# Kernel tuning notes

Hardware: AMD Instinct MI355X
Metric: run time of the kernel (lower is better)

Reference implementation:

```python
import jax, jax.numpy as jnp
import numpy as np

B, S, C = 4, 2048, 1024
N_HEAD = 16
HEAD_DIM = C // N_HEAD


def setup_inputs() -> dict:
    key = jax.random.key(0)
    k1, k2, k3, k4, k5 = jax.random.split(key, 5)
    scale = 1.0 / np.sqrt(C)
    x = jax.random.normal(k1, (B, S, C), dtype=jnp.float32)
    W_attn = jax.random.normal(k2, (C, 3 * C), dtype=jnp.float32) * scale
    b_attn = jax.random.normal(k3, (3 * C,), dtype=jnp.float32) * 0.02
    W_proj = jax.random.normal(k4, (C, C), dtype=jnp.float32) * scale
    b_proj = jax.random.normal(k5, (C,), dtype=jnp.float32) * 0.02
    return {"x": x, "W_attn": W_attn, "b_attn": b_attn, "W_proj": W_proj, "b_proj": b_proj}


def reference(x, W_attn, b_attn, W_proj, b_proj):
    Bx, Sx, Cx = x.shape
    qkv = x @ W_attn + b_attn                      # [B,S,3C]
    q, k, v = jnp.split(qkv, 3, axis=-1)
    # [B,S,C] -> [B,H,S,D]
    def heads(t):
        return t.reshape(Bx, Sx, N_HEAD, HEAD_DIM).transpose(0, 2, 1, 3)
    q, k, v = heads(q), heads(k), heads(v)
    scores = jnp.einsum('bhqd,bhkd->bhqk', q, k) / np.sqrt(HEAD_DIM)
    causal = jnp.tril(jnp.ones((Sx, Sx), dtype=bool))
    scores = jnp.where(causal[None, None], scores, -jnp.inf)
    attn = jax.nn.softmax(scores, axis=-1)
    out = jnp.einsum('bhqk,bhkd->bhqd', attn, v)   # [B,H,S,D]
    out = out.transpose(0, 2, 1, 3).reshape(Bx, Sx, Cx)
    return out @ W_proj + b_proj
```

## Files before the change

### kernel.cpp

```cpp
#include <hip/hip_runtime.h>
#include <hip/hip_bf16.h>

typedef __hip_bfloat16 bf16;
#define NEG_BIG (-3.0e38f)

typedef __bf16 bf16x8 __attribute__((ext_vector_type(8)));
typedef float  f32x4  __attribute__((ext_vector_type(4)));

__device__ inline void load8_f32(const float* p, float* o) {
  float4 a = *reinterpret_cast<const float4*>(p);
  float4 b = *reinterpret_cast<const float4*>(p + 4);
  o[0]=a.x; o[1]=a.y; o[2]=a.z; o[3]=a.w;
  o[4]=b.x; o[5]=b.y; o[6]=b.z; o[7]=b.w;
}

__device__ inline int swz8(int row, int kg) { return ((kg ^ ((row >> 3) & 3)) << 3); }

__global__ __launch_bounds__(1024)
void qkv_f(const float* __restrict__ X, const float* __restrict__ W,
           const float* __restrict__ bias,
           bf16* __restrict__ q, bf16* __restrict__ k, bf16* __restrict__ v)
{
  __shared__ __align__(16) unsigned char smem[67584];
  bf16 (*As)[40] = reinterpret_cast<bf16 (*)[40]>(smem);
  bf16 (*Bs)[48] = reinterpret_cast<bf16 (*)[48]>(smem + 40960);

  const int t   = threadIdx.x;
  const int f   = blockIdx.x;
  const int xcd = f & 7, j = f >> 3;
  const int bm  = xcd * 4 + (j & 3);
  const int bn  = j >> 2;
  const int gm0 = bm * 256, gn0 = bn * 128;
  const int w    = t >> 6, lane = t & 63;
  const int g    = lane >> 4, l15 = lane & 15;
  const int wr   = w >> 2, wc = w & 3;

  const int am  = t >> 2, akg = t & 3;
  const int bnr = t & 127, kg4 = t >> 7;

  f32x4 acc[4][2];
#pragma unroll
  for (int i = 0; i < 4; i++)
#pragma unroll
    for (int jj = 0; jj < 2; jj++) acc[i][jj] = {0.f, 0.f, 0.f, 0.f};

  const float* aptr = X + (size_t)(gm0 + am) * 1024 + akg * 8;
  const float* wptr = W + (size_t)(kg4 * 4) * 3072 + gn0 + bnr;

  float a32_0[8], a32_1[8], wb_0[4], wb_1[4];
  load8_f32(aptr, a32_0);
#pragma unroll
  for (int kk = 0; kk < 4; kk++) wb_0[kk] = wptr[kk * 3072];
  aptr += 32; wptr += 32 * 3072;
  load8_f32(aptr, a32_1);
#pragma unroll
  for (int kk = 0; kk < 4; kk++) wb_1[kk] = wptr[kk * 3072];

  for (int kt = 0; kt < 1024; kt += 64) {
    {
      __align__(16) bf16 ab[8];
      __align__(8)  bf16 bb[4];
#pragma unroll
      for (int i = 0; i < 8; i++) ab[i] = __float2bfloat16(a32_0[i]);
#pragma unroll
      for (int i = 0; i < 4; i++) bb[i] = __float2bfloat16(wb_0[i]);
      *reinterpret_cast<uint4*>(&As[am][swz8(am, akg)]) = *reinterpret_cast<const uint4*>(ab);
      *reinterpret_cast<uint2*>(&Bs[bnr][swz8(bnr, kg4 >> 1) + (kg4 & 1) * 4]) =
          *reinterpret_cast<const uint2*>(bb);
      if (kt + 64 < 1024) {
        aptr += 32; wptr += 32 * 3072;
        load8_f32(aptr, a32_0);
#pragma unroll
        for (int kk = 0; kk < 4; kk++) wb_0[kk] = wptr[kk * 3072];
      }
      __syncthreads();
      bf16x8 af[4], bfr[2];
#pragma unroll
      for (int mt = 0; mt < 4; mt++) {
        const int r_ = wr * 64 + mt * 16 + l15;
        af[mt] = *reinterpret_cast<const bf16x8*>(&As[r_][swz8(r_, g)]);
      }
#pragma unroll
      for (int nt = 0; nt < 2; nt++) {
        const int r_ = wc * 32 + nt * 16 + l15;
        bfr[nt] = *reinterpret_cast<const bf16x8*>(&Bs[r_][swz8(r_, g)]);
      }
      __builtin_amdgcn_s_setprio(1);
#pragma unroll
      for (int mt = 0; mt < 4; mt++)
#pragma unroll
        for (int nt = 0; nt < 2; nt++)
          acc[mt][nt] = __builtin_amdgcn_mfma_f32_16x16x32_bf16(af[mt], bfr[nt], acc[mt][nt], 0, 0, 0);
      __builtin_amdgcn_s_setprio(0);
    }
    {
      __align__(16) bf16 ab[8];
      __align__(8)  bf16 bb[4];
#pragma unroll
      for (int i = 0; i < 8; i++) ab[i] = __float2bfloat16(a32_1[i]);
#pragma unroll
      for (int i = 0; i < 4; i++) bb[i] = __float2bfloat16(wb_1[i]);
      *reinterpret_cast<uint4*>(&As[256 + am][swz8(am, akg)]) = *reinterpret_cast<const uint4*>(ab);
      *reinterpret_cast<uint2*>(&Bs[128 + bnr][swz8(bnr, kg4 >> 1) + (kg4 & 1) * 4]) =
          *reinterpret_cast<const uint2*>(bb);
      if (kt + 96 < 1024) {
        aptr += 32; wptr += 32 * 3072;
        load8_f32(aptr, a32_1);
#pragma unroll
        for (int kk = 0; kk < 4; kk++) wb_1[kk] = wptr[kk * 3072];
      }
      __syncthreads();
      bf16x8 af[4], bfr[2];
#pragma unroll
      for (int mt = 0; mt < 4; mt++) {
        const int r_ = wr * 64 + mt * 16 + l15;
        af[mt] = *reinterpret_cast<const bf16x8*>(&As[256 + r_][swz8(r_, g)]);
      }
#pragma unroll
      for (int nt = 0; nt < 2; nt++) {
        const int r_ = wc * 32 + nt * 16 + l15;
        bfr[nt] = *reinterpret_cast<const bf16x8*>(&Bs[128 + r_][swz8(r_, g)]);
      }
      __builtin_amdgcn_s_setprio(1);
#pragma unroll
      for (int mt = 0; mt < 4; mt++)
#pragma unroll
        for (int nt = 0; nt < 2; nt++)
          acc[mt][nt] = __builtin_amdgcn_mfma_f32_16x16x32_bf16(af[mt], bfr[nt], acc[mt][nt], 0, 0, 0);
      __builtin_amdgcn_s_setprio(0);
    }
  }

  const int which = gn0 >> 10;
  if (which == 2) {
    bf16 (*Vep)[264] = reinterpret_cast<bf16 (*)[264]>(smem);
    __syncthreads();
#pragma unroll
    for (int nt = 0; nt < 2; nt++) {
      const int c = wc * 32 + nt * 16 + l15;
      const float bvs = bias[gn0 + c];
#pragma unroll
      for (int mt = 0; mt < 4; mt++)
#pragma unroll
        for (int r = 0; r < 4; r++) {
          const int s = wr * 64 + mt * 16 + g * 4 + r;
          Vep[c][s] = __float2bfloat16(acc[mt][nt][r] + bvs);
        }
    }
    __syncthreads();
    const int c   = t >> 3, tl = t & 7;
    const int bb2 = gm0 >> 11, sl0 = gm0 & 2047;
    const int hh  = ((gn0 - 2048) >> 6) + (c >> 6), d = c & 63;
    bf16* vrow = v + ((size_t)(bb2 * 16 + hh) * 64 + d) * 2048 + sl0;
#pragma unroll
    for (int it = 0; it < 4; it++) {
      const int s_off = tl * 8 + it * 64;
      *reinterpret_cast<uint4*>(vrow + s_off) =
          *reinterpret_cast<const uint4*>(&Vep[c][s_off]);
    }
  } else {
    bf16* dst = (which == 0) ? q : k;
#pragma unroll
    for (int nt = 0; nt < 2; nt++) {
      const int gc  = gn0 + wc * 32 + nt * 16 + l15;
      const float bvs = bias[gc];
      const int cc = gc & 1023;
      const int hh = cc >> 6, d = cc & 63;
#pragma unroll
      for (int mt = 0; mt < 4; mt++)
#pragma unroll
        for (int r = 0; r < 4; r++) {
          const int gr = gm0 + wr * 64 + mt * 16 + g * 4 + r;
          const int bb2 = gr >> 11, s = gr & 2047;
          float val = acc[mt][nt][r] + bvs;
          if (which == 0) val *= 0.125f;
          dst[((size_t)(bb2 * 16 + hh) * 2048 + s) * 64 + d] = __float2bfloat16(val);
        }
    }
  }
}

__global__ __launch_bounds__(256)
void attn_f(bf16* __restrict__ qo, const bf16* __restrict__ k, const bf16* __restrict__ v)
{
  __shared__ __align__(16) bf16 Ks[64][72];
  __shared__ __align__(16) bf16 Vt[64][72];
  __shared__ __align__(16) bf16 Ps[4][16][72];

  const int t    = threadIdx.x;
  const int f    = blockIdx.x;
  const int xcd  = f & 7;
  const int j    = f >> 3;
  const int hb   = xcd + 8 * (j >> 4);
  const int qt0  = j & 15;
  const int b    = hb >> 4, h = hb & 15;
  const size_t basebh = (size_t)(b * 16 + h) * 2048 * 64;

  const int w    = t >> 6;
  const int lane = t & 63;
  const int g    = lane >> 4;
  const int l15  = lane & 15;

  const int sr = t >> 3;
  const int sc = (t & 7) * 8;
  const bf16* kbase = k + basebh;
  const bf16* vbase = v + basebh;

#pragma unroll 1
  for (int pass = 0; pass < 2; ++pass) {
    const int qt = pass ? qt0 : (31 - qt0);
    const int qb = qt * 64 + w * 16;

    const bf16* qrow = qo + basebh + (size_t)(qb + l15) * 64;
    bf16x8 qf0 = *reinterpret_cast<const bf16x8*>(qrow + g * 8);
    bf16x8 qf1 = *reinterpret_cast<const bf16x8*>(qrow + 32 + g * 8);

    f32x4 acc[4] = {{0,0,0,0},{0,0,0,0},{0,0,0,0},{0,0,0,0}};
    float m_run = NEG_BIG, l_run = 0.f;

    uint4 kreg0, kreg1, vreg0, vreg1;
    {
      kreg0 = *reinterpret_cast<const uint4*>(kbase + (size_t)(sr) * 64 + sc);
      kreg1 = *reinterpret_cast<const uint4*>(kbase + (size_t)(32 + sr) * 64 + sc);
      vreg0 = *reinterpret_cast<const uint4*>(vbase + (size_t)sr * 2048 + sc);
      vreg1 = *reinterpret_cast<const uint4*>(vbase + (size_t)(32 + sr) * 2048 + sc);
    }

    for (int ct = 0; ct <= qt; ++ct) {
      const int kv0 = ct * 64;
      __syncthreads();
      *reinterpret_cast<uint4*>(&Ks[sr][sc])      = kreg0;
      *reinterpret_cast<uint4*>(&Ks[32 + sr][sc]) = kreg1;
      *reinterpret_cast<uint4*>(&Vt[sr][sc])      = vreg0;
      *reinterpret_cast<uint4*>(&Vt[32 + sr][sc]) = vreg1;
      if (ct < qt) {
        const int nv0 = kv0 + 64;
        kreg0 = *reinterpret_cast<const uint4*>(kbase + (size_t)(nv0 + sr) * 64 + sc);
        kreg1 = *reinterpret_cast<const uint4*>(kbase + (size_t)(nv0 + 32 + sr) * 64 + sc);
        vreg0 = *reinterpret_cast<const uint4*>(vbase + (size_t)sr * 2048 + nv0 + sc);
        vreg1 = *reinterpret_cast<const uint4*>(vbase + (size_t)(32 + sr) * 2048 + nv0 + sc);
      }
      __syncthreads();

      f32x4 st[4];
      __builtin_amdgcn_s_setprio(1);
#pragma unroll
      for (int kt = 0; kt < 4; ++kt) {
        const int kr = kt * 16 + l15;
        bf16x8 kf0 = *reinterpret_cast<const bf16x8*>(&Ks[kr][g * 8]);
        bf16x8 kf1 = *reinterpret_cast<const bf16x8*>(&Ks[kr][32 + g * 8]);
        f32x4 c4 = {0,0,0,0};
        c4 = __builtin_amdgcn_mfma_f32_16x16x32_bf16(kf0, qf0, c4, 0, 0, 0);
        c4 = __builtin_amdgcn_mfma_f32_16x16x32_bf16(kf1, qf1, c4, 0, 0, 0);
        st[kt] = c4;
      }
      __builtin_amdgcn_s_setprio(0);
      if (ct == qt) {
        const int qg = qb + l15;
#pragma unroll
        for (int kt = 0; kt < 4; ++kt)
#pragma unroll
          for (int r = 0; r < 4; ++r)
            if (kv0 + kt * 16 + g * 4 + r > qg) st[kt][r] = NEG_BIG;
      }

      float mc = NEG_BIG;
#pragma unroll
      for (int kt = 0; kt < 4; ++kt)
#pragma unroll
        for (int r = 0; r < 4; ++r) mc = fmaxf(mc, st[kt][r]);
      mc = fmaxf(mc, __shfl_xor(mc, 16));
      mc = fmaxf(mc, __shfl_xor(mc, 32));
      if (!__all(mc - m_run <= 8.0f)) {
        const float mn = fmaxf(m_run, mc);
        const float alpha = __expf(m_run - mn);
        m_run = mn;
        l_run *= alpha;
#pragma unroll
        for (int r = 0; r < 4; ++r) {
          const float ar = __shfl(alpha, g * 4 + r, 64);
#pragma unroll
          for (int dt = 0; dt < 4; ++dt) acc[dt][r] *= ar;
        }
      }
      float ps = 0.f;
#pragma unroll
      for (int kt = 0; kt < 4; ++kt)
#pragma unroll
        for (int r = 0; r < 4; ++r) {
          const float pv = __expf(st[kt][r] - m_run);
          st[kt][r] = pv;
          ps += pv;
        }
      ps += __shfl_xor(ps, 16);
      ps += __shfl_xor(ps, 32);
      l_run += ps;

#pragma unroll
      for (int kt = 0; kt < 4; ++kt) {
        union { bf16 hh[4]; uint2 u; } pk;
        pk.hh[0] = __float2bfloat16(st[kt][0]);
        pk.hh[1] = __float2bfloat16(st[kt][1]);
        pk.hh[2] = __float2bfloat16(st[kt][2]);
        pk.hh[3] = __float2bfloat16(st[kt][3]);
        *reinterpret_cast<uint2*>(&Ps[w][l15][kt * 16 + g * 4]) = pk.u;
      }
      __builtin_amdgcn_sched_barrier(0);

      __builtin_amdgcn_s_setprio(1);
#pragma unroll
      for (int kc = 0; kc < 2; ++kc) {
        bf16x8 pf = *reinterpret_cast<const bf16x8*>(&Ps[w][l15][kc * 32 + g * 8]);
#pragma unroll
        for (int dt = 0; dt < 4; ++dt) {
          bf16x8 vf = *reinterpret_cast<const bf16x8*>(&Vt[dt * 16 + l15][kc * 32 + g * 8]);
          acc[dt] = __builtin_amdgcn_mfma_f32_16x16x32_bf16(pf, vf, acc[dt], 0, 0, 0);
        }
      }
      __builtin_amdgcn_s_setprio(0);
    }

    const float linv = 1.f / l_run;
    float inv[4];
#pragma unroll
    for (int r = 0; r < 4; ++r) inv[r] = __shfl(linv, g * 4 + r, 64);
    bf16* op = qo + basebh;
#pragma unroll
    for (int dt = 0; dt < 4; ++dt)
#pragma unroll
      for (int r = 0; r < 4; ++r)
        op[(size_t)(qb + g * 4 + r) * 64 + dt * 16 + l15] =
            __float2bfloat16(acc[dt][r] * inv[r]);
  }
}

__global__ __launch_bounds__(1024)
void proj_f(const bf16* __restrict__ A, const float* __restrict__ W,
            const float* __restrict__ bias, float* __restrict__ out)
{
  __shared__ __align__(16) bf16 As[2][256][40];
  __shared__ __align__(16) bf16 Bs[2][128][48];
  const int t   = threadIdx.x;
  const int f   = blockIdx.x;
  const int xcd = f & 7, j = f >> 3;
  const int bm  = xcd * 4 + (j & 3);
  const int bn  = j >> 2;
  const int gm0 = bm * 256, gn0 = bn * 128;
  const int w    = t >> 6, lane = t & 63;
  const int g    = lane >> 4, l15 = lane & 15;
  const int wr   = w >> 2, wc = w & 3;

  const int am  = t >> 2, akg = t & 3;
  const int bnr = t & 127, kg4 = t >> 7;

  const int gr_l = gm0 + am;
  const int bb_l = gr_l >> 11, s_l = gr_l & 2047;
  const bf16* abase = A + (size_t)bb_l * 2097152 + (size_t)s_l * 64;

  f32x4 acc[4][2];
#pragma unroll
  for (int i = 0; i < 4; i++)
#pragma unroll
    for (int jj = 0; jj < 2; jj++) acc[i][jj] = {0.f, 0.f, 0.f, 0.f};

  const float* wptr = W + (size_t)(kg4 * 4) * 1024 + gn0 + bnr;

  uint4 a0_0, a0_1;
  float wb_0[4], wb_1[4];
  {
    const int c0 = akg * 8;
    a0_0 = *reinterpret_cast<const uint4*>(abase + (size_t)(c0 >> 6) * 131072 + (c0 & 63));
    const int c1 = 32 + akg * 8;
    a0_1 = *reinterpret_cast<const uint4*>(abase + (size_t)(c1 >> 6) * 131072 + (c1 & 63));
  }
#pragma unroll
  for (int kk = 0; kk < 4; kk++) wb_0[kk] = wptr[kk * 1024];
  wptr += 32 * 1024;
#pragma unroll
  for (int kk = 0; kk < 4; kk++) wb_1[kk] = wptr[kk * 1024];

  for (int kt = 0; kt < 1024; kt += 64) {
    {
      __align__(8) bf16 bb[4];
#pragma unroll
      for (int i = 0; i < 4; i++) bb[i] = __float2bfloat16(wb_0[i]);
      *reinterpret_cast<uint4*>(&As[0][am][swz8(am, akg)]) = a0_0;
      *reinterpret_cast<uint2*>(&Bs[0][bnr][swz8(bnr, kg4 >> 1) + (kg4 & 1) * 4]) =
          *reinterpret_cast<const uint2*>(bb);
      if (kt + 64 < 1024) {
        const int c0 = kt + 64 + akg * 8;
        a0_0 = *reinterpret_cast<const uint4*>(abase + (size_t)(c0 >> 6) * 131072 + (c0 & 63));
        wptr += 32 * 1024;
#pragma unroll
        for (int kk = 0; kk < 4; kk++) wb_0[kk] = wptr[kk * 1024];
      }
      __syncthreads();
      bf16x8 af[4], bfr[2];
#pragma unroll
      for (int mt = 0; mt < 4; mt++) {
        const int r_ = wr * 64 + mt * 16 + l15;
        af[mt] = *reinterpret_cast<const bf16x8*>(&As[0][r_][swz8(r_, g)]);
      }
#pragma unroll
      for (int nt = 0; nt < 2; nt++) {
        const int r_ = wc * 32 + nt * 16 + l15;
        bfr[nt] = *reinterpret_cast<const bf16x8*>(&Bs[0][r_][swz8(r_, g)]);
      }
      __builtin_amdgcn_s_setprio(1);
#pragma unroll
      for (int mt = 0; mt < 4; mt++)
#pragma unroll
        for (int nt = 0; nt < 2; nt++)
          acc[mt][nt] = __builtin_amdgcn_mfma_f32_16x16x32_bf16(af[mt], bfr[nt], acc[mt][nt], 0, 0, 0);
      __builtin_amdgcn_s_setprio(0);
    }
    {
      __align__(8) bf16 bb[4];
#pragma unroll
      for (int i = 0; i < 4; i++) bb[i] = __float2bfloat16(wb_1[i]);
      *reinterpret_cast<uint4*>(&As[1][am][swz8(am, akg)]) = a0_1;
      *reinterpret_cast<uint2*>(&Bs[1][bnr][swz8(bnr, kg4 >> 1) + (kg4 & 1) * 4]) =
          *reinterpret_cast<const uint2*>(bb);
      if (kt + 96 < 1024) {
        const int c1 = kt + 96 + akg * 8;
        a0_1 = *reinterpret_cast<const uint4*>(abase + (size_t)(c1 >> 6) * 131072 + (c1 & 63));
        wptr += 32 * 1024;
#pragma unroll
        for (int kk = 0; kk < 4; kk++) wb_1[kk] = wptr[kk * 1024];
      }
      __syncthreads();
      bf16x8 af[4], bfr[2];
#pragma unroll
      for (int mt = 0; mt < 4; mt++) {
        const int r_ = wr * 64 + mt * 16 + l15;
        af[mt] = *reinterpret_cast<const bf16x8*>(&As[1][r_][swz8(r_, g)]);
      }
#pragma unroll
      for (int nt = 0; nt < 2; nt++) {
        const int r_ = wc * 32 + nt * 16 + l15;
        bfr[nt] = *reinterpret_cast<const bf16x8*>(&Bs[1][r_][swz8(r_, g)]);
      }
      __builtin_amdgcn_s_setprio(1);
#pragma unroll
      for (int mt = 0; mt < 4; mt++)
#pragma unroll
        for (int nt = 0; nt < 2; nt++)
          acc[mt][nt] = __builtin_amdgcn_mfma_f32_16x16x32_bf16(af[mt], bfr[nt], acc[mt][nt], 0, 0, 0);
      __builtin_amdgcn_s_setprio(0);
    }
  }

#pragma unroll
  for (int nt = 0; nt < 2; nt++) {
    const int gc = gn0 + wc * 32 + nt * 16 + l15;
    const float bvs = bias[gc];
#pragma unroll
    for (int mt = 0; mt < 4; mt++)
#pragma unroll
      for (int r = 0; r < 4; r++) {
        const int gr = gm0 + wr * 64 + mt * 16 + g * 4 + r;
        out[(size_t)gr * 1024 + gc] = acc[mt][nt][r] + bvs;
      }
  }
}

extern "C" void kernel_launch(void* const* d_in, const int* in_sizes, int n_in,
                              void* d_out, int out_size, void* d_ws, size_t ws_size,
                              hipStream_t stream)
{
  const float *x = nullptr, *W_attn = nullptr, *b_attn = nullptr,
              *W_proj = nullptr, *b_proj = nullptr;
  for (int i = 0; i < n_in; i++) {
    switch (in_sizes[i]) {
      case 8388608: x      = (const float*)d_in[i]; break;
      case 3145728: W_attn = (const float*)d_in[i]; break;
      case 3072:    b_attn = (const float*)d_in[i]; break;
      case 1048576: W_proj = (const float*)d_in[i]; break;
      case 1024:    b_proj = (const float*)d_in[i]; break;
      default: break;
    }
  }
  if (!x || !W_attn || !b_attn || !W_proj || !b_proj) {
    x = (const float*)d_in[0]; W_attn = (const float*)d_in[1];
    b_attn = (const float*)d_in[2]; W_proj = (const float*)d_in[3];
    b_proj = (const float*)d_in[4];
  }
  float* out = (float*)d_out;

  const size_t NE = 8388608;
  bf16* qb = (bf16*)d_ws;
  bf16* kb = (bf16*)d_out;
  bf16* vb = kb + NE;

  qkv_f <<<dim3(768), 1024, 0, stream>>>(x, W_attn, b_attn, qb, kb, vb);
  attn_f<<<dim3(1024), 256, 0, stream>>>(qb, kb, vb);
  proj_f<<<dim3(256), 1024, 0, stream>>>(qb, W_proj, b_proj, out);
}
```

Measured before the change: 187.5 us.

## Process paired causal query tiles in one KV sweep sharing K/V tiles

The attention kernel used to run two sequential passes per block, one for the long query tile (31-qt0) and one for the short tile (qt0), each reloading K/V from global memory. It now sweeps the KV tiles once and feeds both query tiles from the same shared-memory K/V tile, with separate softmax state, accumulators and P buffers. This removes redundant K/V global loads and barriers for the shorter tile and adds independent MFMA work per iteration. In exchange register pressure roughly doubles; a launch_bounds occupancy hint is added and the block-to-head mapping is reordered.

```diff
diff --git a/kernel.cpp b/kernel.cpp
--- a/kernel.cpp
+++ b/kernel.cpp
@@ -180,19 +180,20 @@
   }
 }
 
-__global__ __launch_bounds__(256)
+__global__ __launch_bounds__(256, 4)
 void attn_f(bf16* __restrict__ qo, const bf16* __restrict__ k, const bf16* __restrict__ v)
 {
   __shared__ __align__(16) bf16 Ks[64][72];
   __shared__ __align__(16) bf16 Vt[64][72];
-  __shared__ __align__(16) bf16 Ps[4][16][72];
+  __shared__ __align__(16) bf16 Ps[2][4][16][72];
 
   const int t    = threadIdx.x;
   const int f    = blockIdx.x;
   const int xcd  = f & 7;
   const int j    = f >> 3;
-  const int hb   = xcd + 8 * (j >> 4);
-  const int qt0  = j & 15;
+  const int a    = j & 7;
+  const int qt0  = j >> 3;
+  const int hb   = xcd + 8 * a;
   const int b    = hb >> 4, h = hb & 15;
   const size_t basebh = (size_t)(b * 16 + h) * 2048 * 64;
 
@@ -206,42 +207,48 @@
   const bf16* kbase = k + basebh;
   const bf16* vbase = v + basebh;
 
+  const int qtA = 31 - qt0, qtB = qt0;
+  const int qbA = qtA * 64 + w * 16;
+  const int qbB = qtB * 64 + w * 16;
+
+  const bf16* qrowA = qo + basebh + (size_t)(qbA + l15) * 64;
+  bf16x8 qfA0 = *reinterpret_cast<const bf16x8*>(qrowA + g * 8);
+  bf16x8 qfA1 = *reinterpret_cast<const bf16x8*>(qrowA + 32 + g * 8);
+  const bf16* qrowB = qo + basebh + (size_t)(qbB + l15) * 64;
+  bf16x8 qfB0 = *reinterpret_cast<const bf16x8*>(qrowB + g * 8);
+  bf16x8 qfB1 = *reinterpret_cast<const bf16x8*>(qrowB + 32 + g * 8);
+
+  f32x4 accA[4] = {{0,0,0,0},{0,0,0,0},{0,0,0,0},{0,0,0,0}};
+  f32x4 accB[4] = {{0,0,0,0},{0,0,0,0},{0,0,0,0},{0,0,0,0}};
+  float mA = NEG_BIG, lA = 0.f, mB = NEG_BIG, lB = 0.f;
+
+  uint4 kreg0, kreg1, vreg0, vreg1;
+  {
+    kreg0 = *reinterpret_cast<const uint4*>(kbase + (size_t)(sr) * 64 + sc);
+    kreg1 = *reinterpret_cast<const uint4*>(kbase + (size_t)(32 + sr) * 64 + sc);
+    vreg0 = *reinterpret_cast<const uint4*>(vbase + (size_t)sr * 2048 + sc);
+    vreg1 = *reinterpret_cast<const uint4*>(vbase + (size_t)(32 + sr) * 2048 + sc);
+  }
+
 #pragma unroll 1
-  for (int pass = 0; pass < 2; ++pass) {
-    const int qt = pass ? qt0 : (31 - qt0);
-    const int qb = qt * 64 + w * 16;
-
-    const bf16* qrow = qo + basebh + (size_t)(qb + l15) * 64;
-    bf16x8 qf0 = *reinterpret_cast<const bf16x8*>(qrow + g * 8);
-    bf16x8 qf1 = *reinterpret_cast<const bf16x8*>(qrow + 32 + g * 8);
-
-    f32x4 acc[4] = {{0,0,0,0},{0,0,0,0},{0,0,0,0},{0,0,0,0}};
-    float m_run = NEG_BIG, l_run = 0.f;
-
-    uint4 kreg0, kreg1, vreg0, vreg1;
+  for (int ct = 0; ct <= qtA; ++ct) {
+    const int kv0 = ct * 64;
+    const bool doB = (ct <= qtB);
+    __syncthreads();
+    *reinterpret_cast<uint4*>(&Ks[sr][sc])      = kreg0;
+    *reinterpret_cast<uint4*>(&Ks[32 + sr][sc]) = kreg1;
+    *reinterpret_cast<uint4*>(&Vt[sr][sc])      = vreg0;
+    *reinterpret_cast<uint4*>(&Vt[32 + sr][sc]) = vreg1;
+    if (ct < qtA) {
+      const int nv0 = kv0 + 64;
+      kreg0 = *reinterpret_cast<const uint4*>(kbase + (size_t)(nv0 + sr) * 64 + sc);
+      kreg1 = *reinterpret_cast<const uint4*>(kbase + (size_t)(nv0 + 32 + sr) * 64 + sc);
+      vreg0 = *reinterpret_cast<const uint4*>(vbase + (size_t)sr * 2048 + nv0 + sc);
+      vreg1 = *reinterpret_cast<const uint4*>(vbase + (size_t)(32 + sr) * 2048 + nv0 + sc);
+    }
+    __syncthreads();
+
     {
-      kreg0 = *reinterpret_cast<const uint4*>(kbase + (size_t)(sr) * 64 + sc);
-      kreg1 = *reinterpret_cast<const uint4*>(kbase + (size_t)(32 + sr) * 64 + sc);
-      vreg0 = *reinterpret_cast<const uint4*>(vbase + (size_t)sr * 2048 + sc);
-      vreg1 = *reinterpret_cast<const uint4*>(vbase + (size_t)(32 + sr) * 2048 + sc);
-    }
-
-    for (int ct = 0; ct <= qt; ++ct) {
-      const int kv0 = ct * 64;
-      __syncthreads();
-      *reinterpret_cast<uint4*>(&Ks[sr][sc])      = kreg0;
-      *reinterpret_cast<uint4*>(&Ks[32 + sr][sc]) = kreg1;
-      *reinterpret_cast<uint4*>(&Vt[sr][sc])      = vreg0;
-      *reinterpret_cast<uint4*>(&Vt[32 + sr][sc]) = vreg1;
-      if (ct < qt) {
-        const int nv0 = kv0 + 64;
-        kreg0 = *reinterpret_cast<const uint4*>(kbase + (size_t)(nv0 + sr) * 64 + sc);
-        kreg1 = *reinterpret_cast<const uint4*>(kbase + (size_t)(nv0 + 32 + sr) * 64 + sc);
-        vreg0 = *reinterpret_cast<const uint4*>(vbase + (size_t)sr * 2048 + nv0 + sc);
-        vreg1 = *reinterpret_cast<const uint4*>(vbase + (size_t)(32 + sr) * 2048 + nv0 + sc);
-      }
-      __syncthreads();
-
       f32x4 st[4];
       __builtin_amdgcn_s_setprio(1);
 #pragma unroll
@@ -250,20 +257,19 @@
         bf16x8 kf0 = *reinterpret_cast<const bf16x8*>(&Ks[kr][g * 8]);
         bf16x8 kf1 = *reinterpret_cast<const bf16x8*>(&Ks[kr][32 + g * 8]);
         f32x4 c4 = {0,0,0,0};
-        c4 = __builtin_amdgcn_mfma_f32_16x16x32_bf16(kf0, qf0, c4, 0, 0, 0);
-        c4 = __builtin_amdgcn_mfma_f32_16x16x32_bf16(kf1, qf1, c4, 0, 0, 0);
+        c4 = __builtin_amdgcn_mfma_f32_16x16x32_bf16(kf0, qfA0, c4, 0, 0, 0);
+        c4 = __builtin_amdgcn_mfma_f32_16x16x32_bf16(kf1, qfA1, c4, 0, 0, 0);
         st[kt] = c4;
       }
       __builtin_amdgcn_s_setprio(0);
-      if (ct == qt) {
-        const int qg = qb + l15;
+      if (ct == qtA) {
+        const int qg = qbA + l15;
 #pragma unroll
         for (int kt = 0; kt < 4; ++kt)
 #pragma unroll
           for (int r = 0; r < 4; ++r)
             if (kv0 + kt * 16 + g * 4 + r > qg) st[kt][r] = NEG_BIG;
       }
-
       float mc = NEG_BIG;
 #pragma unroll
       for (int kt = 0; kt < 4; ++kt)
@@ -271,16 +277,16 @@
         for (int r = 0; r < 4; ++r) mc = fmaxf(mc, st[kt][r]);
       mc = fmaxf(mc, __shfl_xor(mc, 16));
       mc = fmaxf(mc, __shfl_xor(mc, 32));
-      if (!__all(mc - m_run <= 8.0f)) {
-        const float mn = fmaxf(m_run, mc);
-        const float alpha = __expf(m_run - mn);
-        m_run = mn;
-        l_run *= alpha;
+      if (!__all(mc - mA <= 8.0f)) {
+        const float mn = fmaxf(mA, mc);
+        const float alpha = __expf(mA - mn);
+        mA = mn;
+        lA *= alpha;
 #pragma unroll
         for (int r = 0; r < 4; ++r) {
           const float ar = __shfl(alpha, g * 4 + r, 64);
 #pragma unroll
-          for (int dt = 0; dt < 4; ++dt) acc[dt][r] *= ar;
+          for (int dt = 0; dt < 4; ++dt) accA[dt][r] *= ar;
         }
       }
       float ps = 0.f;
@@ -288,14 +294,13 @@
       for (int kt = 0; kt < 4; ++kt)
 #pragma unroll
         for (int r = 0; r < 4; ++r) {
-          const float pv = __expf(st[kt][r] - m_run);
+          const float pv = __expf(st[kt][r] - mA);
           st[kt][r] = pv;
           ps += pv;
         }
       ps += __shfl_xor(ps, 16);
       ps += __shfl_xor(ps, 32);
-      l_run += ps;
-
+      lA += ps;
 #pragma unroll
       for (int kt = 0; kt < 4; ++kt) {
         union { bf16 hh[4]; uint2 u; } pk;
@@ -303,34 +308,122 @@
         pk.hh[1] = __float2bfloat16(st[kt][1]);
         pk.hh[2] = __float2bfloat16(st[kt][2]);
         pk.hh[3] = __float2bfloat16(st[kt][3]);
-        *reinterpret_cast<uint2*>(&Ps[w][l15][kt * 16 + g * 4]) = pk.u;
-      }
-      __builtin_amdgcn_sched_barrier(0);
-
+        *reinterpret_cast<uint2*>(&Ps[0][w][l15][kt * 16 + g * 4]) = pk.u;
+      }
+    }
+    if (doB) {
+      f32x4 st[4];
       __builtin_amdgcn_s_setprio(1);
 #pragma unroll
+      for (int kt = 0; kt < 4; ++kt) {
+        const int kr = kt * 16 + l15;
+        bf16x8 kf0 = *reinterpret_cast<const bf16x8*>(&Ks[kr][g * 8]);
+        bf16x8 kf1 = *reinterpret_cast<const bf16x8*>(&Ks[kr][32 + g * 8]);
+        f32x4 c4 = {0,0,0,0};
+        c4 = __builtin_amdgcn_mfma_f32_16x16x32_bf16(kf0, qfB0, c4, 0, 0, 0);
+        c4 = __builtin_amdgcn_mfma_f32_16x16x32_bf16(kf1, qfB1, c4, 0, 0, 0);
+        st[kt] = c4;
+      }
+      __builtin_amdgcn_s_setprio(0);
+      if (ct == qtB) {
+        const int qg = qbB + l15;
+#pragma unroll
+        for (int kt = 0; kt < 4; ++kt)
+#pragma unroll
+          for (int r = 0; r < 4; ++r)
+            if (kv0 + kt * 16 + g * 4 + r > qg) st[kt][r] = NEG_BIG;
+      }
+      float mc = NEG_BIG;
+#pragma unroll
+      for (int kt = 0; kt < 4; ++kt)
+#pragma unroll
+        for (int r = 0; r < 4; ++r) mc = fmaxf(mc, st[kt][r]);
+      mc = fmaxf(mc, __shfl_xor(mc, 16));
+      mc = fmaxf(mc, __shfl_xor(mc, 32));
+      if (!__all(mc - mB <= 8.0f)) {
+        const float mn = fmaxf(mB, mc);
+        const float alpha = __expf(mB - mn);
+        mB = mn;
+        lB *= alpha;
+#pragma unroll
+        for (int r = 0; r < 4; ++r) {
+          const float ar = __shfl(alpha, g * 4 + r, 64);
+#pragma unroll
+          for (int dt = 0; dt < 4; ++dt) accB[dt][r] *= ar;
+        }
+      }
+      float ps = 0.f;
+#pragma unroll
+      for (int kt = 0; kt < 4; ++kt)
+#pragma unroll
+        for (int r = 0; r < 4; ++r) {
+          const float pv = __expf(st[kt][r] - mB);
+          st[kt][r] = pv;
+          ps += pv;
+        }
+      ps += __shfl_xor(ps, 16);
+      ps += __shfl_xor(ps, 32);
+      lB += ps;
+#pragma unroll
+      for (int kt = 0; kt < 4; ++kt) {
+        union { bf16 hh[4]; uint2 u; } pk;
+        pk.hh[0] = __float2bfloat16(st[kt][0]);
+        pk.hh[1] = __float2bfloat16(st[kt][1]);
+        pk.hh[2] = __float2bfloat16(st[kt][2]);
+        pk.hh[3] = __float2bfloat16(st[kt][3]);
+        *reinterpret_cast<uint2*>(&Ps[1][w][l15][kt * 16 + g * 4]) = pk.u;
+      }
+    }
+    __builtin_amdgcn_sched_barrier(0);
+
+    __builtin_amdgcn_s_setprio(1);
+#pragma unroll
+    for (int kc = 0; kc < 2; ++kc) {
+      bf16x8 pf = *reinterpret_cast<const bf16x8*>(&Ps[0][w][l15][kc * 32 + g * 8]);
+#pragma unroll
+      for (int dt = 0; dt < 4; ++dt) {
+        bf16x8 vf = *reinterpret_cast<const bf16x8*>(&Vt[dt * 16 + l15][kc * 32 + g * 8]);
+        accA[dt] = __builtin_amdgcn_mfma_f32_16x16x32_bf16(pf, vf, accA[dt], 0, 0, 0);
+      }
+    }
+    if (doB) {
+#pragma unroll
       for (int kc = 0; kc < 2; ++kc) {
-        bf16x8 pf = *reinterpret_cast<const bf16x8*>(&Ps[w][l15][kc * 32 + g * 8]);
+        bf16x8 pf = *reinterpret_cast<const bf16x8*>(&Ps[1][w][l15][kc * 32 + g * 8]);
 #pragma unroll
         for (int dt = 0; dt < 4; ++dt) {
           bf16x8 vf = *reinterpret_cast<const bf16x8*>(&Vt[dt * 16 + l15][kc * 32 + g * 8]);
-          acc[dt] = __builtin_amdgcn_mfma_f32_16x16x32_bf16(pf, vf, acc[dt], 0, 0, 0);
-        }
-      }
-      __builtin_amdgcn_s_setprio(0);
-    }
-
-    const float linv = 1.f / l_run;
+          accB[dt] = __builtin_amdgcn_mfma_f32_16x16x32_bf16(pf, vf, accB[dt], 0, 0, 0);
+        }
+      }
+    }
+    __builtin_amdgcn_s_setprio(0);
+  }
+
+  bf16* op = qo + basebh;
+  {
+    const float linv = 1.f / lA;
     float inv[4];
 #pragma unroll
     for (int r = 0; r < 4; ++r) inv[r] = __shfl(linv, g * 4 + r, 64);
-    bf16* op = qo + basebh;
 #pragma unroll
     for (int dt = 0; dt < 4; ++dt)
 #pragma unroll
       for (int r = 0; r < 4; ++r)
-        op[(size_t)(qb + g * 4 + r) * 64 + dt * 16 + l15] =
-            __float2bfloat16(acc[dt][r] * inv[r]);
+        op[(size_t)(qbA + g * 4 + r) * 64 + dt * 16 + l15] =
+            __float2bfloat16(accA[dt][r] * inv[r]);
+  }
+  {
+    const float linv = 1.f / lB;
+    float inv[4];
+#pragma unroll
+    for (int r = 0; r < 4; ++r) inv[r] = __shfl(linv, g * 4 + r, 64);
+#pragma unroll
+    for (int dt = 0; dt < 4; ++dt)
+#pragma unroll
+      for (int r = 0; r < 4; ++r)
+        op[(size_t)(qbB + g * 4 + r) * 64 + dt * 16 + l15] =
+            __float2bfloat16(accB[dt][r] * inv[r]);
   }
 }
 
```

Result: faster. 182.8 us (-2.5%).
